# Kernel tuning notes

Hardware: AMD Instinct MI355X
Metric: run time of the kernel (lower is better)

The kernel has to match this reference:

```python
import jax, jax.numpy as jnp
import numpy as np

B = 16384
S = 7          # grid cells per side
C = 30         # 2 boxes * 5 + 20 classes
GX = 7.0       # num_gridx = labels.shape[-2]
GY = 30.0      # num_gridy = labels.shape[-1]  (faithful to the original code's size()[-2:] bug)


def setup_inputs() -> dict:
    key = jax.random.key(0)
    k1, k2, k3 = jax.random.split(key, 3)
    # keep w,h away from 0 so sqrt grads are finite
    pred = jax.random.uniform(k1, (B, S, S, C), dtype=jnp.float32, minval=0.05, maxval=0.95)
    labels = jax.random.uniform(k2, (B, S, S, C), dtype=jnp.float32, minval=0.05, maxval=0.95)
    obj = jax.random.bernoulli(k3, 0.3, (B, S, S)).astype(jnp.float32)
    labels = labels.at[..., 4].set(obj)
    return {"pred": pred, "labels": labels}


def _boxes_xyxy(t, off, mg, ng):
    # t[..., off:off+4] = (x, y, w, h) relative to cell; convert to xyxy
    cx = (t[..., off] + mg) / GX
    cy = (t[..., off + 1] + ng) / GY
    w = t[..., off + 2]
    h = t[..., off + 3]
    return jnp.stack([cx - w / 2, cy - h / 2, cx + w / 2, cy + h / 2], axis=-1)


def _iou(b1, b2):
    ix1 = jnp.maximum(b1[..., 0], b2[..., 0])
    iy1 = jnp.maximum(b1[..., 1], b2[..., 1])
    ix2 = jnp.minimum(b1[..., 2], b2[..., 2])
    iy2 = jnp.minimum(b1[..., 3], b2[..., 3])
    iw = jnp.maximum(ix2 - ix1, 0.0)
    ih = jnp.maximum(iy2 - iy1, 0.0)
    inter = iw * ih
    a1 = (b1[..., 2] - b1[..., 0]) * (b1[..., 3] - b1[..., 1])
    a2 = (b2[..., 2] - b2[..., 0]) * (b2[..., 3] - b2[..., 1])
    union = a1 + a2 - inter
    pos = inter > 0
    return jnp.where(pos, inter / jnp.where(pos, union, 1.0), 0.0)


def reference(pred, labels):
    n_batch = pred.shape[0]
    # grid offsets: m indexes axis 1, n indexes axis 2
    mg = jnp.arange(S, dtype=pred.dtype)[:, None]   # (7,1)
    ng = jnp.arange(S, dtype=pred.dtype)[None, :]   # (1,7)

    pb1 = _boxes_xyxy(pred, 0, mg, ng)
    pb2 = _boxes_xyxy(pred, 5, mg, ng)
    gb = _boxes_xyxy(labels, 0, mg, ng)
    iou1 = _iou(pb1, gb)   # (B,7,7)
    iou2 = _iou(pb2, gb)
    sel1 = iou1 >= iou2
    obj = labels[..., 4] == 1.0

    coor1 = (jnp.sum((pred[..., 0:2] - labels[..., 0:2]) ** 2, -1)
             + jnp.sum((jnp.sqrt(pred[..., 2:4]) - jnp.sqrt(labels[..., 2:4])) ** 2, -1))
    coor2 = (jnp.sum((pred[..., 5:7] - labels[..., 5:7]) ** 2, -1)
             + jnp.sum((jnp.sqrt(pred[..., 7:9]) - jnp.sqrt(labels[..., 7:9])) ** 2, -1))
    coor = 5.0 * jnp.where(sel1, coor1, coor2)

    d1 = (pred[..., 4] - iou1) ** 2
    d2 = (pred[..., 9] - iou2) ** 2
    obj_confi = jnp.where(sel1, d1, d2)
    noobj_at_obj = 0.5 * jnp.where(sel1, d2, d1)

    class_loss = jnp.sum((pred[..., 10:] - labels[..., 10:]) ** 2, -1)

    noobj_at_noobj = 0.5 * (pred[..., 4] ** 2 + pred[..., 9] ** 2)

    per_cell = jnp.where(obj, coor + obj_confi + noobj_at_obj + class_loss, noobj_at_noobj)
    return jnp.sum(per_cell) / n_batch
```

## Files before the change

kernel.cpp:

```cpp
#include <hip/hip_runtime.h>


#define NCELLS (16384 * 49)
#define INV_NB (1.0f / 16384.0f)

__device__ __forceinline__ float iou_xyxy(float ax1, float ay1, float ax2, float ay2,
                                          float bx1, float by1, float bx2, float by2) {
    float ix1 = fmaxf(ax1, bx1);
    float iy1 = fmaxf(ay1, by1);
    float ix2 = fminf(ax2, bx2);
    float iy2 = fminf(ay2, by2);
    float iw = fmaxf(ix2 - ix1, 0.0f);
    float ih = fmaxf(iy2 - iy1, 0.0f);
    float inter = iw * ih;
    float a1 = (ax2 - ax1) * (ay2 - ay1);
    float a2 = (bx2 - bx1) * (by2 - by1);
    float uni = a1 + a2 - inter;
    return (inter > 0.0f) ? (inter / uni) : 0.0f;
}

__global__ __launch_bounds__(256) void yolo_loss_kernel(const float* __restrict__ pred,
                                                        const float* __restrict__ labels,
                                                        float* __restrict__ out) {
    int cell = blockIdx.x * blockDim.x + threadIdx.x;

    float per = 0.0f;
    if (cell < NCELLS) {
        int rem = cell % 49;
        float fm = (float)(rem / 7);
        float fn = (float)(rem % 7);

        const float2* p2 = reinterpret_cast<const float2*>(pred + (size_t)cell * 30);
        const float2* l2 = reinterpret_cast<const float2*>(labels + (size_t)cell * 30);

        float pv[30], lv[30];
#pragma unroll
        for (int k = 0; k < 15; ++k) {
            float2 a = p2[k];
            pv[2 * k] = a.x; pv[2 * k + 1] = a.y;
        }
#pragma unroll
        for (int k = 0; k < 15; ++k) {
            float2 b = l2[k];
            lv[2 * k] = b.x; lv[2 * k + 1] = b.y;
        }

        float cx = (pv[0] + fm) / 7.0f;
        float cy = (pv[1] + fn) / 30.0f;
        float w = pv[2], h = pv[3];
        float p1x1 = cx - w * 0.5f, p1y1 = cy - h * 0.5f;
        float p1x2 = cx + w * 0.5f, p1y2 = cy + h * 0.5f;
        cx = (pv[5] + fm) / 7.0f;
        cy = (pv[6] + fn) / 30.0f;
        w = pv[7]; h = pv[8];
        float p2x1 = cx - w * 0.5f, p2y1 = cy - h * 0.5f;
        float p2x2 = cx + w * 0.5f, p2y2 = cy + h * 0.5f;
        cx = (lv[0] + fm) / 7.0f;
        cy = (lv[1] + fn) / 30.0f;
        w = lv[2]; h = lv[3];
        float gx1 = cx - w * 0.5f, gy1 = cy - h * 0.5f;
        float gx2 = cx + w * 0.5f, gy2 = cy + h * 0.5f;

        float iou1 = iou_xyxy(p1x1, p1y1, p1x2, p1y2, gx1, gy1, gx2, gy2);
        float iou2 = iou_xyxy(p2x1, p2y1, p2x2, p2y2, gx1, gy1, gx2, gy2);

        bool sel1 = (iou1 >= iou2);
        bool obj = (lv[4] == 1.0f);

        float dx = pv[0] - lv[0], dy = pv[1] - lv[1];
        float dw = sqrtf(pv[2]) - sqrtf(lv[2]);
        float dh = sqrtf(pv[3]) - sqrtf(lv[3]);
        float coor1 = dx * dx + dy * dy + dw * dw + dh * dh;

        dx = pv[5] - lv[5]; dy = pv[6] - lv[6];
        dw = sqrtf(pv[7]) - sqrtf(lv[7]);
        dh = sqrtf(pv[8]) - sqrtf(lv[8]);
        float coor2 = dx * dx + dy * dy + dw * dw + dh * dh;

        float coor = 5.0f * (sel1 ? coor1 : coor2);

        float d1 = pv[4] - iou1; d1 *= d1;
        float d2 = pv[9] - iou2; d2 *= d2;
        float obj_confi = sel1 ? d1 : d2;
        float noobj_at_obj = 0.5f * (sel1 ? d2 : d1);

        float cls = 0.0f;
#pragma unroll
        for (int k = 10; k < 30; ++k) {
            float d = pv[k] - lv[k];
            cls += d * d;
        }

        float noobj_at_noobj = 0.5f * (pv[4] * pv[4] + pv[9] * pv[9]);

        per = obj ? (coor + obj_confi + noobj_at_obj + cls) : noobj_at_noobj;
    }

    float acc = per;
#pragma unroll
    for (int off = 32; off > 0; off >>= 1) acc += __shfl_down(acc, off, 64);

    __shared__ float sbuf[4];
    int lane = threadIdx.x & 63;
    int wid = threadIdx.x >> 6;
    if (lane == 0) sbuf[wid] = acc;
    __syncthreads();
    if (threadIdx.x == 0) {
        float s = (sbuf[0] + sbuf[1] + sbuf[2] + sbuf[3]) * INV_NB;
        atomicAdd(out, s);
    }
}

extern "C" void kernel_launch(void* const* d_in, const int* in_sizes, int n_in,
                              void* d_out, int out_size, void* d_ws, size_t ws_size,
                              hipStream_t stream) {
    const float* pred = (const float*)d_in[0];
    const float* labels = (const float*)d_in[1];
    float* out = (float*)d_out;

    hipMemsetAsync(out, 0, sizeof(float), stream);

    const int threads = 256;
    const int blocks = (NCELLS + threads - 1) / threads;
    yolo_loss_kernel<<<blocks, threads, 0, stream>>>(pred, labels, out);
}
```

Before: 206.3 us.

## Stage pred and labels tiles through shared memory with coalesced float4 loads

Each block now loads its contiguous 256-cell slices of pred and labels into LDS using fully coalesced float4 loads, then each thread reads its 30-float record from shared memory. This replaces the strided per-thread float2 global loads, which touched many cache lines per wavefront. It relies on NCELLS being divisible by 256 and drops the bounds check. It uses 60 KB of LDS per block, which caps occupancy, and the launch bounds now request 2 blocks per CU.

```diff
diff --git a/kernel.cpp b/kernel.cpp
--- a/kernel.cpp
+++ b/kernel.cpp
@@ -3,6 +3,9 @@
 
 #define NCELLS (16384 * 49)
 #define INV_NB (1.0f / 16384.0f)
+#define CPB 256
+#define FPA (CPB * 30)
+#define F4PA (FPA / 4)
 
 __device__ __forceinline__ float iou_xyxy(float ax1, float ay1, float ax2, float ay2,
                                           float bx1, float by1, float bx2, float by2) {
@@ -19,93 +22,108 @@
     return (inter > 0.0f) ? (inter / uni) : 0.0f;
 }
 
-__global__ __launch_bounds__(256) void yolo_loss_kernel(const float* __restrict__ pred,
-                                                        const float* __restrict__ labels,
-                                                        float* __restrict__ out) {
-    int cell = blockIdx.x * blockDim.x + threadIdx.x;
+__global__ __launch_bounds__(256, 2) void yolo_loss_kernel(const float* __restrict__ pred,
+                                                           const float* __restrict__ labels,
+                                                           float* __restrict__ out) {
+    __shared__ float sm[2 * FPA];
 
-    float per = 0.0f;
-    if (cell < NCELLS) {
-        int rem = cell % 49;
-        float fm = (float)(rem / 7);
-        float fn = (float)(rem % 7);
+    const int t = threadIdx.x;
+    const float* gp = pred + (size_t)blockIdx.x * FPA;
+    const float* gl = labels + (size_t)blockIdx.x * FPA;
 
-        const float2* p2 = reinterpret_cast<const float2*>(pred + (size_t)cell * 30);
-        const float2* l2 = reinterpret_cast<const float2*>(labels + (size_t)cell * 30);
+    float4* sm4 = reinterpret_cast<float4*>(sm);
+    const float4* gp4 = reinterpret_cast<const float4*>(gp);
+    const float4* gl4 = reinterpret_cast<const float4*>(gl);
+#pragma unroll
+    for (int i = 0; i < 15; ++i) {
+        int idx = i * 256 + t;
+        float4 v = (idx < F4PA) ? gp4[idx] : gl4[idx - F4PA];
+        sm4[idx] = v;
+    }
+    __syncthreads();
 
-        float pv[30], lv[30];
+    const int gcell = blockIdx.x * CPB + t;
+    const int rem = gcell % 49;
+    const float fm = (float)(rem / 7);
+    const float fn = (float)(rem % 7);
+
+    const float2* ps = reinterpret_cast<const float2*>(sm + t * 30);
+    const float2* ls = reinterpret_cast<const float2*>(sm + FPA + t * 30);
+
+    float pv[30], lv[30];
 #pragma unroll
-        for (int k = 0; k < 15; ++k) {
-            float2 a = p2[k];
-            pv[2 * k] = a.x; pv[2 * k + 1] = a.y;
-        }
+    for (int k = 0; k < 15; ++k) {
+        float2 a = ps[k];
+        pv[2 * k] = a.x; pv[2 * k + 1] = a.y;
+    }
 #pragma unroll
-        for (int k = 0; k < 15; ++k) {
-            float2 b = l2[k];
-            lv[2 * k] = b.x; lv[2 * k + 1] = b.y;
-        }
+    for (int k = 0; k < 15; ++k) {
+        float2 b = ls[k];
+        lv[2 * k] = b.x; lv[2 * k + 1] = b.y;
+    }
 
-        float cx = (pv[0] + fm) / 7.0f;
-        float cy = (pv[1] + fn) / 30.0f;
-        float w = pv[2], h = pv[3];
-        float p1x1 = cx - w * 0.5f, p1y1 = cy - h * 0.5f;
-        float p1x2 = cx + w * 0.5f, p1y2 = cy + h * 0.5f;
-        cx = (pv[5] + fm) / 7.0f;
-        cy = (pv[6] + fn) / 30.0f;
-        w = pv[7]; h = pv[8];
-        float p2x1 = cx - w * 0.5f, p2y1 = cy - h * 0.5f;
-        float p2x2 = cx + w * 0.5f, p2y2 = cy + h * 0.5f;
-        cx = (lv[0] + fm) / 7.0f;
-        cy = (lv[1] + fn) / 30.0f;
-        w = lv[2]; h = lv[3];
-        float gx1 = cx - w * 0.5f, gy1 = cy - h * 0.5f;
-        float gx2 = cx + w * 0.5f, gy2 = cy + h * 0.5f;
+    float cx = (pv[0] + fm) / 7.0f;
+    float cy = (pv[1] + fn) / 30.0f;
+    float w = pv[2], h = pv[3];
+    float p1x1 = cx - w * 0.5f, p1y1 = cy - h * 0.5f;
+    float p1x2 = cx + w * 0.5f, p1y2 = cy + h * 0.5f;
 
-        float iou1 = iou_xyxy(p1x1, p1y1, p1x2, p1y2, gx1, gy1, gx2, gy2);
-        float iou2 = iou_xyxy(p2x1, p2y1, p2x2, p2y2, gx1, gy1, gx2, gy2);
+    cx = (pv[5] + fm) / 7.0f;
+    cy = (pv[6] + fn) / 30.0f;
+    w = pv[7]; h = pv[8];
+    float p2x1 = cx - w * 0.5f, p2y1 = cy - h * 0.5f;
+    float p2x2 = cx + w * 0.5f, p2y2 = cy + h * 0.5f;
 
-        bool sel1 = (iou1 >= iou2);
-        bool obj = (lv[4] == 1.0f);
+    cx = (lv[0] + fm) / 7.0f;
+    cy = (lv[1] + fn) / 30.0f;
+    w = lv[2]; h = lv[3];
+    float gx1 = cx - w * 0.5f, gy1 = cy - h * 0.5f;
+    float gx2 = cx + w * 0.5f, gy2 = cy + h * 0.5f;
 
-        float dx = pv[0] - lv[0], dy = pv[1] - lv[1];
-        float dw = sqrtf(pv[2]) - sqrtf(lv[2]);
-        float dh = sqrtf(pv[3]) - sqrtf(lv[3]);
-        float coor1 = dx * dx + dy * dy + dw * dw + dh * dh;
+    float iou1 = iou_xyxy(p1x1, p1y1, p1x2, p1y2, gx1, gy1, gx2, gy2);
+    float iou2 = iou_xyxy(p2x1, p2y1, p2x2, p2y2, gx1, gy1, gx2, gy2);
 
-        dx = pv[5] - lv[5]; dy = pv[6] - lv[6];
-        dw = sqrtf(pv[7]) - sqrtf(lv[7]);
-        dh = sqrtf(pv[8]) - sqrtf(lv[8]);
-        float coor2 = dx * dx + dy * dy + dw * dw + dh * dh;
+    bool sel1 = (iou1 >= iou2);
+    bool obj = (lv[4] == 1.0f);
 
-        float coor = 5.0f * (sel1 ? coor1 : coor2);
+    float dx = pv[0] - lv[0], dy = pv[1] - lv[1];
+    float dw = sqrtf(pv[2]) - sqrtf(lv[2]);
+    float dh = sqrtf(pv[3]) - sqrtf(lv[3]);
+    float coor1 = dx * dx + dy * dy + dw * dw + dh * dh;
 
-        float d1 = pv[4] - iou1; d1 *= d1;
-        float d2 = pv[9] - iou2; d2 *= d2;
-        float obj_confi = sel1 ? d1 : d2;
-        float noobj_at_obj = 0.5f * (sel1 ? d2 : d1);
+    dx = pv[5] - lv[5]; dy = pv[6] - lv[6];
+    dw = sqrtf(pv[7]) - sqrtf(lv[7]);
+    dh = sqrtf(pv[8]) - sqrtf(lv[8]);
+    float coor2 = dx * dx + dy * dy + dw * dw + dh * dh;
 
-        float cls = 0.0f;
+    float coor = 5.0f * (sel1 ? coor1 : coor2);
+
+    float d1 = pv[4] - iou1; d1 *= d1;
+    float d2 = pv[9] - iou2; d2 *= d2;
+    float obj_confi = sel1 ? d1 : d2;
+    float noobj_at_obj = 0.5f * (sel1 ? d2 : d1);
+
+    float cls = 0.0f;
 #pragma unroll
-        for (int k = 10; k < 30; ++k) {
-            float d = pv[k] - lv[k];
-            cls += d * d;
-        }
+    for (int k = 10; k < 30; ++k) {
+        float d = pv[k] - lv[k];
+        cls += d * d;
+    }
 
-        float noobj_at_noobj = 0.5f * (pv[4] * pv[4] + pv[9] * pv[9]);
+    float noobj_at_noobj = 0.5f * (pv[4] * pv[4] + pv[9] * pv[9]);
 
-        per = obj ? (coor + obj_confi + noobj_at_obj + cls) : noobj_at_noobj;
-    }
+    float per = obj ? (coor + obj_confi + noobj_at_obj + cls) : noobj_at_noobj;
 
     float acc = per;
 #pragma unroll
     for (int off = 32; off > 0; off >>= 1) acc += __shfl_down(acc, off, 64);
 
     __shared__ float sbuf[4];
-    int lane = threadIdx.x & 63;
-    int wid = threadIdx.x >> 6;
+    int lane = t & 63;
+    int wid = t >> 6;
     if (lane == 0) sbuf[wid] = acc;
     __syncthreads();
-    if (threadIdx.x == 0) {
+    if (t == 0) {
         float s = (sbuf[0] + sbuf[1] + sbuf[2] + sbuf[3]) * INV_NB;
         atomicAdd(out, s);
     }
@@ -121,6 +139,6 @@
     hipMemsetAsync(out, 0, sizeof(float), stream);
 
     const int threads = 256;
-    const int blocks = (NCELLS + threads - 1) / threads;
+    const int blocks = NCELLS / threads;
     yolo_loss_kernel<<<blocks, threads, 0, stream>>>(pred, labels, out);
 }
```

New measurement: 204.0 us. About the same (-1.1%).
